# Kernel tuning notes

Hardware: AMD Instinct MI355X
Metric: run time of the kernel (lower is better)

Reference implementation:

```python
import jax, jax.numpy as jnp
import numpy as np

EPS_GN = 1e-5
EPS_ATTN = 1e-6
HEADS = 4
DIM_HEAD = 32
GROUPS = 32  # min(32, channels=128)


def group_norm(x, weight, bias, groups=GROUPS, eps=EPS_GN):
    # x: [b, c, h, w]
    b, c, h, w = x.shape
    xg = x.reshape(b, groups, c // groups, h, w)
    mean = xg.mean(axis=(2, 3, 4), keepdims=True)
    var = xg.var(axis=(2, 3, 4), keepdims=True)
    xg = (xg - mean) * jax.lax.rsqrt(var + eps)
    x = xg.reshape(b, c, h, w)
    return x * weight[None, :, None, None] + bias[None, :, None, None]


def conv1x1(x, w):
    # x: [b, c, h, w], w: [out, in] -> [b, out, h, w]
    return jnp.einsum('bchw,oc->bohw', x, w)


def setup_inputs() -> dict:
    key = jax.random.key(0)
    ks = jax.random.split(key, 6)
    b, c, h, w = 16, 128, 128, 128
    inner = HEADS * DIM_HEAD  # 128
    x = jax.random.normal(ks[0], (b, c, h, w), dtype=jnp.float32)
    gn1_w = jnp.ones((c,), jnp.float32) + 0.02 * jax.random.normal(ks[1], (c,), jnp.float32)
    gn1_b = 0.02 * jax.random.normal(ks[2], (c,), jnp.float32)
    w_qkv = jax.random.normal(ks[3], (inner * 3, c), jnp.float32) / np.sqrt(c)
    w_out = jax.random.normal(ks[4], (c, inner), jnp.float32) / np.sqrt(inner)
    gn2_w = jnp.ones((c,), jnp.float32) + 0.02 * jax.random.normal(ks[5], (c,), jnp.float32)
    gn2_b = jnp.zeros((c,), jnp.float32)
    return {"x": x, "gn1_w": gn1_w, "gn1_b": gn1_b, "w_qkv": w_qkv,
            "w_out": w_out, "gn2_w": gn2_w, "gn2_b": gn2_b}


def reference(x, gn1_w, gn1_b, w_qkv, w_out, gn2_w, gn2_b):
    b, c, h, w = x.shape
    residual = x
    xn = group_norm(x, gn1_w, gn1_b)
    qkv = conv1x1(xn, w_qkv)                      # [b, 3*inner, h, w]
    q, k, v = jnp.split(qkv, 3, axis=1)
    # 'b (heads d) h w -> b heads (h w) d'
    def to_tokens(t):
        return t.reshape(b, HEADS, DIM_HEAD, h * w).transpose(0, 1, 3, 2)
    q, k, v = to_tokens(q), to_tokens(k), to_tokens(v)
    q = jax.nn.elu(q) + 1.0
    k = jax.nn.elu(k) + 1.0
    k_sum = k.sum(axis=2)                          # [b, heads, d]
    kv = jnp.einsum('bhnd,bhne->bhde', k, v)       # [b, heads, d, d]
    qk_sum = jnp.einsum('bhnd,bhd->bhn', q, k_sum) # [b, heads, n]
    qkv_out = jnp.einsum('bhnd,bhde->bhne', q, kv) # [b, heads, n, d]
    out = qkv_out / (qk_sum[..., None] + EPS_ATTN)
    # 'b heads (h w) d -> b (heads d) h w'
    out = out.transpose(0, 1, 3, 2).reshape(b, HEADS * DIM_HEAD, h, w)
    out = conv1x1(out, w_out)
    out = group_norm(out, gn2_w, gn2_b)
    return out + residual
```

## Files before the change

### kernel.cpp

```cpp
#include <hip/hip_runtime.h>

#define B_   16
#define C_   128
#define HW_  16384

typedef __attribute__((ext_vector_type(4))) float  floatx4;
typedef __attribute__((ext_vector_type(8))) short  short8;
typedef __attribute__((ext_vector_type(4))) short  short4v;

static __device__ __forceinline__ unsigned short f2bf(float f){
  unsigned int u = __float_as_uint(f);
  u += 0x7FFFu + ((u >> 16) & 1u);
  return (unsigned short)(u >> 16);
}
static __device__ __forceinline__ float bf2f(unsigned short h){
  return __uint_as_float(((unsigned int)h) << 16);
}
static __device__ __forceinline__ float elu1(float v){
  return v > 0.f ? v + 1.f : __expf(v);
}
static __device__ __forceinline__ int keyx(int n){ return ((n >> 1) & 7) ^ ((n >> 4) & 7); }

__global__ __launch_bounds__(512) void k_xprep(const float* __restrict__ x,
    unsigned short* __restrict__ xT, float* __restrict__ gn1part){
  int blk = blockIdx.x;
  int b = blk >> 6, tile = blk & 63;
  int n0 = tile * 256;
  __shared__ unsigned short XS[32768];
  int t = threadIdx.x, w = t >> 6, l = t & 63;
  float sk[4], sk2[4];
  #pragma unroll
  for (int k = 0; k < 4; ++k){ sk[k] = 0.f; sk2[k] = 0.f; }
  #pragma unroll
  for (int k = 0; k < 4; ++k){
    float4 f4[4];
    #pragma unroll
    for (int j = 0; j < 4; ++j){
      int c = 16*w + 4*k + j;
      f4[j] = *(const float4*)(x + ((size_t)(b*128 + c))*HW_ + n0 + 4*l);
    }
    #pragma unroll
    for (int j = 0; j < 4; ++j){
      sk[k]  += f4[j].x + f4[j].y + f4[j].z + f4[j].w;
      sk2[k] += f4[j].x*f4[j].x + f4[j].y*f4[j].y + f4[j].z*f4[j].z + f4[j].w*f4[j].w;
    }
    int c0 = 16*w + 4*k, cs = c0 >> 3, co = c0 & 7;
    #pragma unroll
    for (int i = 0; i < 4; ++i){
      int n = 4*l + i;
      short4v p;
      #pragma unroll
      for (int j = 0; j < 4; ++j) p[j] = (short)f2bf(((const float*)&f4[j])[i]);
      *(short4v*)(XS + n*128 + (((cs ^ keyx(n)) << 3) + co)) = p;
    }
  }
  #pragma unroll
  for (int k = 0; k < 4; ++k){
    float a = sk[k], q = sk2[k];
    #pragma unroll
    for (int o = 32; o; o >>= 1){ a += __shfl_down(a, o); q += __shfl_down(q, o); }
    if (l == 0){
      gn1part[((size_t)blk)*64 + (4*w + k)*2 + 0] = a;
      gn1part[((size_t)blk)*64 + (4*w + k)*2 + 1] = q;
    }
  }
  __syncthreads();
  unsigned short* dst = xT + ((size_t)blk)*32768;
  for (int it = 0; it < 8; ++it){
    int slot = t + it*512;
    *(short8*)(dst + slot*8) = *(const short8*)(XS + slot*8);
  }
}

__global__ __launch_bounds__(64) void k_gn1fin(const float* __restrict__ gn1part,
    float* __restrict__ mean, float* __restrict__ rstd){
  int bg = blockIdx.x;
  int b = bg >> 5, g = bg & 31, l = threadIdx.x;
  const float* p = gn1part + ((size_t)(b*64 + l))*64 + g*2;
  float s = p[0], s2 = p[1];
  #pragma unroll
  for (int o = 32; o; o >>= 1){ s += __shfl_down(s, o); s2 += __shfl_down(s2, o); }
  if (l == 0){
    float m = s * (1.f/65536.f);
    float var = s2 * (1.f/65536.f) - m*m;
    mean[bg] = m; rstd[bg] = rsqrtf(var + 1e-5f);
  }
}

__global__ __launch_bounds__(64) void k_fold(const float* __restrict__ wqkv, const float* __restrict__ wout,
    const float* __restrict__ g1w, const float* __restrict__ g1b,
    const float* __restrict__ mean, const float* __restrict__ rstd,
    unsigned short* __restrict__ wqp, float* __restrict__ bias, unsigned short* __restrict__ woutb){
  int i = blockIdx.x, l = threadIdx.x;
  if (i < 6144){
    int b = i / 384, o = i % 384;
    float bsum = 0.f;
    #pragma unroll
    for (int j = 0; j < 2; ++j){
      int c = l*2 + j, g = c >> 2;
      float m = mean[b*32 + g], r = rstd[b*32 + g];
      float A  = r * g1w[c];
      float Bc = g1b[c] - m * A;
      float wv = wqkv[o*128 + c];
      wqp[((size_t)(b*384 + o))*128 + c] = f2bf(wv * A);
      bsum += wv * Bc;
    }
    #pragma unroll
    for (int o2 = 32; o2; o2 >>= 1) bsum += __shfl_down(bsum, o2);
    if (l == 0) bias[b*384 + o] = bsum;
  } else {
    int r = i - 6144;
    #pragma unroll
    for (int j = 0; j < 2; ++j){ int c = l*2 + j; woutb[r*128 + c] = f2bf(wout[r*128 + c]); }
  }
}

__global__ __launch_bounds__(512) void k_kv(const unsigned short* __restrict__ xT,
    const unsigned short* __restrict__ wqp, const float* __restrict__ bias,
    float* __restrict__ kvpart, float* __restrict__ ksumpart){
  int blk = blockIdx.x;
  int b = blk >> 7, nt = blk & 127;
  __shared__ unsigned short S[32768];
  int t = threadIdx.x, w = t >> 6, lane = t & 63, lr = lane & 15, lk = lane >> 4;
  const unsigned short* src = xT + ((size_t)(b*64 + (nt >> 1)))*32768 + (nt & 1)*16384;
  for (int it = 0; it < 4; ++it){
    int slot = t + it*512;
    *(short8*)(S + slot*8) = *(const short8*)(src + slot*8);
  }
  __syncthreads();
  short8 afr[2][4]; float biasr[2][4];
  #pragma unroll
  for (int rt = 0; rt < 2; ++rt){
    int o = 128 + rt*128 + w*16;
    #pragma unroll
    for (int ks = 0; ks < 4; ++ks)
      afr[rt][ks] = *(const short8*)(wqp + ((size_t)(b*384 + o + lr))*128 + ks*32 + lk*8);
    #pragma unroll
    for (int r = 0; r < 4; ++r) biasr[rt][r] = bias[b*384 + o + lk*4 + r];
  }
  short4v kpk[8], vpk[8];
  for (int ct = 0; ct < 8; ++ct){
    int nr = ct*16 + lr;
    int kn = keyx(nr);
    short8 bfr[4];
    #pragma unroll
    for (int ks = 0; ks < 4; ++ks)
      bfr[ks] = *(const short8*)(S + nr*128 + (((ks*4 + lk) ^ kn) << 3));
    #pragma unroll
    for (int rt = 0; rt < 2; ++rt){
      floatx4 acc = {0.f,0.f,0.f,0.f};
      #pragma unroll
      for (int ks = 0; ks < 4; ++ks)
        acc = __builtin_amdgcn_mfma_f32_16x16x32_bf16(afr[rt][ks], bfr[ks], acc, 0,0,0);
      short4v pk;
      #pragma unroll
      for (int r = 0; r < 4; ++r){
        float v = acc[r] + biasr[rt][r];
        if (rt == 0) v = elu1(v);
        pk[r] = (short)f2bf(v);
      }
      if (rt == 0) kpk[ct] = pk; else vpk[ct] = pk;
    }
  }
  __syncthreads();
  for (int ct = 0; ct < 8; ++ct){
    int n = ct*16 + lr;
    #pragma unroll
    for (int r = 0; r < 4; ++r){
      int c = w*16 + lk*4 + r;
      int key = (c >> 1) & 7;
      int off = c*128 + ((((n >> 3) ^ key) << 3) + (n & 7));
      S[off]         = (unsigned short)kpk[ct][r];
      S[16384 + off] = (unsigned short)vpk[ct][r];
    }
  }
  __syncthreads();
  short8 ones;
  #pragma unroll
  for (int j = 0; j < 8; ++j) ones[j] = (short)0x3F80;
  #pragma unroll
  for (int j = 0; j < 2; ++j){
    int m = w + 8*j;
    int h = m >> 2, dt = (m >> 1) & 1, et = m & 1;
    int arow = h*32 + dt*16 + lr, brow = h*32 + et*16 + lr;
    int akey = (lr >> 1) & 7;
    floatx4 acc = {0.f,0.f,0.f,0.f}, ks_acc = {0.f,0.f,0.f,0.f};
    #pragma unroll
    for (int ks = 0; ks < 4; ++ks){
      short8 ka = *(const short8*)(S + arow*128 + (((ks*4 + lk) ^ akey) << 3));
      short8 vb = *(const short8*)(S + 16384 + brow*128 + (((ks*4 + lk) ^ akey) << 3));
      acc = __builtin_amdgcn_mfma_f32_16x16x32_bf16(ka, vb, acc, 0,0,0);
      if (et == 0) ks_acc = __builtin_amdgcn_mfma_f32_16x16x32_bf16(ka, ones, ks_acc, 0,0,0);
    }
    float* kvp = kvpart + ((size_t)((b*128 + nt)*4 + h))*1024;
    #pragma unroll
    for (int r = 0; r < 4; ++r)
      kvp[(dt*16 + lk*4 + r)*32 + et*16 + lr] = acc[r];
    if (et == 0 && lr == 0){
      float* ksp = ksumpart + ((size_t)((b*128 + nt)*4 + h))*32;
      #pragma unroll
      for (int r = 0; r < 4; ++r) ksp[dt*16 + lk*4 + r] = ks_acc[r];
    }
  }
}

__global__ __launch_bounds__(256) void k_kvmfold(const float* __restrict__ kvpart, const float* __restrict__ ksumpart,
    const unsigned short* __restrict__ woutb, unsigned short* __restrict__ Mb, float* __restrict__ ksumF){
  int bh = blockIdx.x, t = threadIdx.x;
  int b = bh >> 2, h = bh & 3;
  __shared__ float kvL[1024];
  for (int i = t; i < 1024; i += 256){
    float s = 0.f;
    for (int nt = 0; nt < 128; ++nt) s += kvpart[((size_t)((b*128 + nt)*4 + h))*1024 + i];
    kvL[i] = s;
  }
  if (t < 32){
    float s = 0.f;
    for (int nt = 0; nt < 128; ++nt) s += ksumpart[((size_t)((b*128 + nt)*4 + h))*32 + t];
    ksumF[b*128 + h*32 + t] = s;
  }
  __syncthreads();
  int o = t >> 1, d0 = (t & 1)*16;
  float w2row[32];
  #pragma unroll
  for (int e = 0; e < 32; ++e) w2row[e] = bf2f(woutb[o*128 + h*32 + e]);
  for (int dd = 0; dd < 16; ++dd){
    int d = d0 + dd;
    float s = 0.f;
    #pragma unroll
    for (int e = 0; e < 32; ++e) s += w2row[e] * kvL[d*32 + e];
    Mb[((size_t)b)*16384 + o*128 + h*32 + d] = f2bf(s);
  }
}

__global__ __launch_bounds__(512) void k_attn2(const unsigned short* __restrict__ xT,
    const unsigned short* __restrict__ wqp, const float* __restrict__ bias,
    const float* __restrict__ ksumF, const unsigned short* __restrict__ Mb,
    unsigned short* __restrict__ hbT, float* __restrict__ gn2part){
  int blk = blockIdx.x;
  int b = blk >> 6;
  __shared__ unsigned short S[32768];
  int t = threadIdx.x, w = t >> 6, lane = t & 63, lr = lane & 15, lk = lane >> 4;
  int rg = w & 3, cg = w >> 2;
  const unsigned short* src = xT + ((size_t)blk)*32768;
  for (int it = 0; it < 8; ++it){
    int slot = t + it*512;
    *(short8*)(S + slot*8) = *(const short8*)(src + slot*8);
  }
  short8 afr[2][4]; float biasq[2][4], ksL[2][4];
  #pragma unroll
  for (int rtl = 0; rtl < 2; ++rtl){
    int o = rg*32 + rtl*16;
    #pragma unroll
    for (int ks = 0; ks < 4; ++ks)
      afr[rtl][ks] = *(const short8*)(wqp + ((size_t)(b*384 + o + lr))*128 + ks*32 + lk*8);
    #pragma unroll
    for (int r = 0; r < 4; ++r){
      biasq[rtl][r] = bias[b*384 + o + lk*4 + r];
      ksL[rtl][r]   = ksumF[b*128 + o + lk*4 + r];
    }
  }
  __syncthreads();
  short4v qpk[2][8];
  for (int ct = 0; ct < 8; ++ct){
    int nr = cg*128 + ct*16 + lr;
    int kn = keyx(nr);
    short8 bfr[4];
    #pragma unroll
    for (int ks = 0; ks < 4; ++ks)
      bfr[ks] = *(const short8*)(S + nr*128 + (((ks*4 + lk) ^ kn) << 3));
    float qv[2][4];
    #pragma unroll
    for (int rtl = 0; rtl < 2; ++rtl){
      floatx4 acc = {0.f,0.f,0.f,0.f};
      #pragma unroll
      for (int ks = 0; ks < 4; ++ks)
        acc = __builtin_amdgcn_mfma_f32_16x16x32_bf16(afr[rtl][ks], bfr[ks], acc, 0,0,0);
      #pragma unroll
      for (int r = 0; r < 4; ++r) qv[rtl][r] = elu1(acc[r] + biasq[rtl][r]);
    }
    float p = 0.f;
    #pragma unroll
    for (int rtl = 0; rtl < 2; ++rtl)
      #pragma unroll
      for (int r = 0; r < 4; ++r) p += ksL[rtl][r] * qv[rtl][r];
    p += __shfl_xor(p, 16);
    p += __shfl_xor(p, 32);
    float inv = 1.f / (p + 1e-6f);
    #pragma unroll
    for (int rtl = 0; rtl < 2; ++rtl){
      short4v pk;
      #pragma unroll
      for (int r = 0; r < 4; ++r) pk[r] = (short)f2bf(qv[rtl][r] * inv);
      qpk[rtl][ct] = pk;
    }
  }
  short8 afr2[4];
  #pragma unroll
  for (int ks = 0; ks < 4; ++ks)
    afr2[ks] = *(const short8*)(Mb + ((size_t)b)*16384 + (size_t)(w*16 + lr)*128 + ks*32 + lk*8);
  __syncthreads();
  #pragma unroll
  for (int rtl = 0; rtl < 2; ++rtl){
    int c0 = rg*32 + rtl*16 + lk*4;
    #pragma unroll
    for (int ct = 0; ct < 8; ++ct){
      int n = cg*128 + ct*16 + lr;
      *(short4v*)(S + n*128 + ((((c0 >> 3) ^ (n & 7)) << 3) + (c0 & 7))) = qpk[rtl][ct];
    }
  }
  __syncthreads();
  unsigned short* hdst = hbT + ((size_t)blk)*32768;
  float gs[4] = {0,0,0,0}, gq[4] = {0,0,0,0};
  for (int ct = 0; ct < 16; ++ct){
    int nr = ct*16 + lr;
    short8 bfr[4];
    #pragma unroll
    for (int ks = 0; ks < 4; ++ks)
      bfr[ks] = *(const short8*)(S + nr*128 + (((ks*4 + lk) ^ (nr & 7)) << 3));
    floatx4 acc = {0.f,0.f,0.f,0.f};
    #pragma unroll
    for (int ks = 0; ks < 4; ++ks)
      acc = __builtin_amdgcn_mfma_f32_16x16x32_bf16(afr2[ks], bfr[ks], acc, 0,0,0);
    short4v pk;
    #pragma unroll
    for (int r = 0; r < 4; ++r){
      float hv = acc[r];
      pk[r] = (short)f2bf(hv);
      gs[r] += hv; gq[r] += hv*hv;
    }
    *(short4v*)(hdst + (w*16 + ct)*256 + lane*4) = pk;
  }
  #pragma unroll
  for (int m = 1; m < 16; m <<= 1)
    #pragma unroll
    for (int r = 0; r < 4; ++r){ gs[r] += __shfl_xor(gs[r], m); gq[r] += __shfl_xor(gq[r], m); }
  if (lr == 0){
    #pragma unroll
    for (int r = 0; r < 4; ++r){
      int c = w*16 + lk*4 + r;
      gn2part[((size_t)blk*128 + c)*2 + 0] = gs[r];
      gn2part[((size_t)blk*128 + c)*2 + 1] = gq[r];
    }
  }
}

__global__ __launch_bounds__(64) void k_gn2stats(const float* __restrict__ gn2part,
    float* __restrict__ mean, float* __restrict__ rstd){
  int b = blockIdx.x >> 5, g = blockIdx.x & 31;
  int lane = threadIdx.x;
  float s = 0.f, s2 = 0.f;
  #pragma unroll
  for (int j = 0; j < 4; ++j){
    const float* p = gn2part + (((size_t)(b*64 + lane))*128 + g*4 + j)*2;
    s += p[0]; s2 += p[1];
  }
  #pragma unroll
  for (int o = 32; o; o >>= 1){ s += __shfl_down(s, o); s2 += __shfl_down(s2, o); }
  if (lane == 0){
    float m = s * (1.f/65536.f);
    float var = s2 * (1.f/65536.f) - m*m;
    mean[blockIdx.x] = m; rstd[blockIdx.x] = rsqrtf(var + 1e-5f);
  }
}

__global__ __launch_bounds__(256) void k_final(const unsigned short* __restrict__ hbT,
    const unsigned short* __restrict__ xT, float* __restrict__ out,
    const float* __restrict__ mean, const float* __restrict__ rstd,
    const float* __restrict__ g2w, const float* __restrict__ g2b){
  int blk = blockIdx.x;
  int b = blk >> 7, t128 = blk & 127;
  int tile = t128 >> 1, half = t128 & 1;
  __shared__ unsigned short HS[16384];
  __shared__ unsigned short XS[16384];
  int t = threadIdx.x;
  const unsigned short* hsrc = hbT + ((size_t)(b*64 + tile))*32768;
  const unsigned short* xsrc = xT + ((size_t)(b*64 + tile))*32768 + half*16384;
  for (int it = 0; it < 8; ++it){
    int slot = t + it*256;
    int w8 = slot >> 8, rest = slot & 255;
    *(short8*)(HS + slot*8) = *(const short8*)(hsrc + ((w8*16 + half*8)*256 + rest*8));
    *(short8*)(XS + slot*8) = *(const short8*)(xsrc + slot*8);
  }
  __syncthreads();
  for (int it = 0; it < 8; ++it){
    int idx = t + it*256;
    int c = idx >> 4, oct = idx & 15;
    int bg = b*32 + (c >> 2);
    float m = mean[bg], r = rstd[bg];
    float sc = r * g2w[c], sh = g2b[c] - m * sc;
    int hbase0 = ((c >> 4)*8 + (oct >> 1))*256 + ((c >> 2) & 3)*64 + (oct & 1)*32 + (c & 3);
    float ov[8];
    #pragma unroll
    for (int j = 0; j < 8; ++j){
      int n = oct*8 + j;
      float hv = bf2f(HS[hbase0 + j*4]);
      unsigned short xv = XS[n*128 + ((((c >> 3) ^ keyx(n)) << 3) + (c & 7))];
      ov[j] = hv*sc + sh + bf2f(xv);
    }
    float* op = out + ((size_t)(b*128 + c))*HW_ + t128*128 + oct*8;
    float4 o0, o1;
    o0.x = ov[0]; o0.y = ov[1]; o0.z = ov[2]; o0.w = ov[3];
    o1.x = ov[4]; o1.y = ov[5]; o1.z = ov[6]; o1.w = ov[7];
    *(float4*)op = o0; *(float4*)(op + 4) = o1;
  }
}

extern "C" void kernel_launch(void* const* d_in, const int* in_sizes, int n_in,
                              void* d_out, int out_size, void* d_ws, size_t ws_size,
                              hipStream_t stream){
  const float* x    = (const float*)d_in[0];
  const float* g1w  = (const float*)d_in[1];
  const float* g1b  = (const float*)d_in[2];
  const float* wqkv = (const float*)d_in[3];
  const float* wout = (const float*)d_in[4];
  const float* g2w  = (const float*)d_in[5];
  const float* g2b  = (const float*)d_in[6];
  char* ws = (char*)d_ws;
  (void)in_sizes; (void)n_in; (void)out_size; (void)ws_size;

  float* gn1part  = (float*)(ws + 0);
  float* gn1_mean = (float*)(ws + 262144);
  float* gn1_rstd = (float*)(ws + 264192);
  float* gn2_mean = (float*)(ws + 266240);
  float* gn2_rstd = (float*)(ws + 268288);
  float* bias     = (float*)(ws + 270336);
  unsigned short* woutb = (unsigned short*)(ws + 294912);
  float* ksumF    = (float*)(ws + 327680);
  unsigned short* Mb = (unsigned short*)(ws + 335872);
  unsigned short* wqp = (unsigned short*)(ws + 860160);
  float* ksumpart = (float*)(ws + 2433024);
  float* kvpart   = (float*)(ws + 4194304);
  float* gn2part  = (float*)(ws + 37748736);
  unsigned short* xT  = (unsigned short*)(ws + 46137344);
  unsigned short* hbT = (unsigned short*)(ws + 113246208);

  k_xprep<<<dim3(1024), dim3(512), 0, stream>>>(x, xT, gn1part);
  k_gn1fin<<<dim3(512), dim3(64), 0, stream>>>(gn1part, gn1_mean, gn1_rstd);
  k_fold<<<dim3(6272), dim3(64), 0, stream>>>(wqkv, wout, g1w, g1b, gn1_mean, gn1_rstd, wqp, bias, woutb);
  k_kv<<<dim3(2048), dim3(512), 0, stream>>>(xT, wqp, bias, kvpart, ksumpart);
  k_kvmfold<<<dim3(64), dim3(256), 0, stream>>>(kvpart, ksumpart, woutb, Mb, ksumF);
  k_attn2<<<dim3(1024), dim3(512), 0, stream>>>(xT, wqp, bias, ksumF, Mb, hbT, gn2part);
  k_gn2stats<<<dim3(512), dim3(64), 0, stream>>>(gn2part, gn2_mean, gn2_rstd);
  k_final<<<dim3(2048), dim3(256), 0, stream>>>(hbT, xT, (float*)d_out, gn2_mean, gn2_rstd, g2w, g2b);
}
```

Baseline: 216.5 us.

## Process two token halves per k_kv block and retile attn2 output projection

k_kv now handles a full 256-token tile per block, looping over two halves and accumulating kv and ksum in registers. This halves the grid and the partial buffers that k_kvmfold must reduce. The MFMA operand order is swapped so results are written to LDS as packed short4 stores instead of scalar stores. In k_attn2 each wave now computes two 16-channel row tiles over half the tokens, reusing each LDS B-fragment for two MFMAs. gn2 partials are split by cg, and k_gn2stats is updated to match.

```diff
diff --git a/kernel.cpp b/kernel.cpp
--- a/kernel.cpp
+++ b/kernel.cpp
@@ -119,87 +119,97 @@
     const unsigned short* __restrict__ wqp, const float* __restrict__ bias,
     float* __restrict__ kvpart, float* __restrict__ ksumpart){
   int blk = blockIdx.x;
-  int b = blk >> 7, nt = blk & 127;
+  int b = blk >> 6;
   __shared__ unsigned short S[32768];
   int t = threadIdx.x, w = t >> 6, lane = t & 63, lr = lane & 15, lk = lane >> 4;
-  const unsigned short* src = xT + ((size_t)(b*64 + (nt >> 1)))*32768 + (nt & 1)*16384;
-  for (int it = 0; it < 4; ++it){
-    int slot = t + it*512;
-    *(short8*)(S + slot*8) = *(const short8*)(src + slot*8);
-  }
-  __syncthreads();
-  short8 afr[2][4]; float biasr[2][4];
+  short8 wfr[2][4]; float biasv[2];
   #pragma unroll
   for (int rt = 0; rt < 2; ++rt){
     int o = 128 + rt*128 + w*16;
     #pragma unroll
     for (int ks = 0; ks < 4; ++ks)
-      afr[rt][ks] = *(const short8*)(wqp + ((size_t)(b*384 + o + lr))*128 + ks*32 + lk*8);
-    #pragma unroll
-    for (int r = 0; r < 4; ++r) biasr[rt][r] = bias[b*384 + o + lk*4 + r];
-  }
-  short4v kpk[8], vpk[8];
-  for (int ct = 0; ct < 8; ++ct){
-    int nr = ct*16 + lr;
-    int kn = keyx(nr);
-    short8 bfr[4];
-    #pragma unroll
-    for (int ks = 0; ks < 4; ++ks)
-      bfr[ks] = *(const short8*)(S + nr*128 + (((ks*4 + lk) ^ kn) << 3));
-    #pragma unroll
-    for (int rt = 0; rt < 2; ++rt){
-      floatx4 acc = {0.f,0.f,0.f,0.f};
+      wfr[rt][ks] = *(const short8*)(wqp + ((size_t)(b*384 + o + lr))*128 + ks*32 + lk*8);
+    biasv[rt] = bias[b*384 + o + lr];
+  }
+  short8 ones;
+  #pragma unroll
+  for (int j = 0; j < 8; ++j) ones[j] = (short)0x3F80;
+  floatx4 accA = {0,0,0,0}, accB = {0,0,0,0}, ksaA = {0,0,0,0}, ksaB = {0,0,0,0};
+  for (int half = 0; half < 2; ++half){
+    const unsigned short* src = xT + ((size_t)blk)*32768 + half*16384;
+    for (int it = 0; it < 4; ++it){
+      int slot = t + it*512;
+      *(short8*)(S + slot*8) = *(const short8*)(src + slot*8);
+    }
+    __syncthreads();
+    short4v kpk[8], vpk[8];
+    for (int ct = 0; ct < 8; ++ct){
+      int nr = ct*16 + lr;
+      int kn = keyx(nr);
+      short8 xfr[4];
       #pragma unroll
       for (int ks = 0; ks < 4; ++ks)
-        acc = __builtin_amdgcn_mfma_f32_16x16x32_bf16(afr[rt][ks], bfr[ks], acc, 0,0,0);
-      short4v pk;
-      #pragma unroll
-      for (int r = 0; r < 4; ++r){
-        float v = acc[r] + biasr[rt][r];
-        if (rt == 0) v = elu1(v);
-        pk[r] = (short)f2bf(v);
+        xfr[ks] = *(const short8*)(S + nr*128 + (((ks*4 + lk) ^ kn) << 3));
+      #pragma unroll
+      for (int rt = 0; rt < 2; ++rt){
+        floatx4 acc = {0.f,0.f,0.f,0.f};
+        #pragma unroll
+        for (int ks = 0; ks < 4; ++ks)
+          acc = __builtin_amdgcn_mfma_f32_16x16x32_bf16(xfr[ks], wfr[rt][ks], acc, 0,0,0);
+        short4v pk;
+        #pragma unroll
+        for (int r = 0; r < 4; ++r){
+          float v = acc[r] + biasv[rt];
+          if (rt == 0) v = elu1(v);
+          pk[r] = (short)f2bf(v);
+        }
+        if (rt == 0) kpk[ct] = pk; else vpk[ct] = pk;
       }
-      if (rt == 0) kpk[ct] = pk; else vpk[ct] = pk;
-    }
-  }
-  __syncthreads();
-  for (int ct = 0; ct < 8; ++ct){
-    int n = ct*16 + lr;
-    #pragma unroll
-    for (int r = 0; r < 4; ++r){
-      int c = w*16 + lk*4 + r;
-      int key = (c >> 1) & 7;
-      int off = c*128 + ((((n >> 3) ^ key) << 3) + (n & 7));
-      S[off]         = (unsigned short)kpk[ct][r];
-      S[16384 + off] = (unsigned short)vpk[ct][r];
-    }
-  }
-  __syncthreads();
-  short8 ones;
-  #pragma unroll
-  for (int j = 0; j < 8; ++j) ones[j] = (short)0x3F80;
+    }
+    __syncthreads();
+    #pragma unroll
+    for (int ct = 0; ct < 8; ++ct){
+      int cimg = w*16 + lr;
+      int n0 = ct*16 + lk*4;
+      int off = cimg*128 + ((((n0 >> 3) ^ ((cimg >> 1) & 7)) << 3) + (n0 & 7));
+      *(short4v*)(S + off)         = kpk[ct];
+      *(short4v*)(S + 16384 + off) = vpk[ct];
+    }
+    __syncthreads();
+    #pragma unroll
+    for (int j = 0; j < 2; ++j){
+      int m = w + 8*j;
+      int h = m >> 2, dt = (m >> 1) & 1, et = m & 1;
+      int arow = h*32 + dt*16 + lr, brow = h*32 + et*16 + lr;
+      int akey = (lr >> 1) & 7;
+      #pragma unroll
+      for (int ks = 0; ks < 4; ++ks){
+        short8 ka = *(const short8*)(S + arow*128 + (((ks*4 + lk) ^ akey) << 3));
+        short8 vb = *(const short8*)(S + 16384 + brow*128 + (((ks*4 + lk) ^ akey) << 3));
+        if (j == 0){
+          accA = __builtin_amdgcn_mfma_f32_16x16x32_bf16(ka, vb, accA, 0,0,0);
+          if (et == 0) ksaA = __builtin_amdgcn_mfma_f32_16x16x32_bf16(ka, ones, ksaA, 0,0,0);
+        } else {
+          accB = __builtin_amdgcn_mfma_f32_16x16x32_bf16(ka, vb, accB, 0,0,0);
+          if (et == 0) ksaB = __builtin_amdgcn_mfma_f32_16x16x32_bf16(ka, ones, ksaB, 0,0,0);
+        }
+      }
+    }
+    __syncthreads();
+  }
   #pragma unroll
   for (int j = 0; j < 2; ++j){
     int m = w + 8*j;
     int h = m >> 2, dt = (m >> 1) & 1, et = m & 1;
-    int arow = h*32 + dt*16 + lr, brow = h*32 + et*16 + lr;
-    int akey = (lr >> 1) & 7;
-    floatx4 acc = {0.f,0.f,0.f,0.f}, ks_acc = {0.f,0.f,0.f,0.f};
-    #pragma unroll
-    for (int ks = 0; ks < 4; ++ks){
-      short8 ka = *(const short8*)(S + arow*128 + (((ks*4 + lk) ^ akey) << 3));
-      short8 vb = *(const short8*)(S + 16384 + brow*128 + (((ks*4 + lk) ^ akey) << 3));
-      acc = __builtin_amdgcn_mfma_f32_16x16x32_bf16(ka, vb, acc, 0,0,0);
-      if (et == 0) ks_acc = __builtin_amdgcn_mfma_f32_16x16x32_bf16(ka, ones, ks_acc, 0,0,0);
-    }
-    float* kvp = kvpart + ((size_t)((b*128 + nt)*4 + h))*1024;
+    floatx4 acc = j ? accB : accA, ksa = j ? ksaB : ksaA;
+    float* kvp = kvpart + ((size_t)(blk*4 + h))*1024;
     #pragma unroll
     for (int r = 0; r < 4; ++r)
       kvp[(dt*16 + lk*4 + r)*32 + et*16 + lr] = acc[r];
     if (et == 0 && lr == 0){
-      float* ksp = ksumpart + ((size_t)((b*128 + nt)*4 + h))*32;
-      #pragma unroll
-      for (int r = 0; r < 4; ++r) ksp[dt*16 + lk*4 + r] = ks_acc[r];
+      float* ksp = ksumpart + ((size_t)(blk*4 + h))*32;
+      #pragma unroll
+      for (int r = 0; r < 4; ++r) ksp[dt*16 + lk*4 + r] = ksa[r];
     }
   }
 }
@@ -211,12 +221,12 @@
   __shared__ float kvL[1024];
   for (int i = t; i < 1024; i += 256){
     float s = 0.f;
-    for (int nt = 0; nt < 128; ++nt) s += kvpart[((size_t)((b*128 + nt)*4 + h))*1024 + i];
+    for (int nt = 0; nt < 64; ++nt) s += kvpart[((size_t)((b*64 + nt)*4 + h))*1024 + i];
     kvL[i] = s;
   }
   if (t < 32){
     float s = 0.f;
-    for (int nt = 0; nt < 128; ++nt) s += ksumpart[((size_t)((b*128 + nt)*4 + h))*32 + t];
+    for (int nt = 0; nt < 64; ++nt) s += ksumpart[((size_t)((b*64 + nt)*4 + h))*32 + t];
     ksumF[b*128 + h*32 + t] = s;
   }
   __syncthreads();
@@ -295,10 +305,12 @@
       qpk[rtl][ct] = pk;
     }
   }
-  short8 afr2[4];
-  #pragma unroll
-  for (int ks = 0; ks < 4; ++ks)
-    afr2[ks] = *(const short8*)(Mb + ((size_t)b)*16384 + (size_t)(w*16 + lr)*128 + ks*32 + lk*8);
+  short8 afr2[2][4];
+  #pragma unroll
+  for (int rtl = 0; rtl < 2; ++rtl)
+    #pragma unroll
+    for (int ks = 0; ks < 4; ++ks)
+      afr2[rtl][ks] = *(const short8*)(Mb + ((size_t)b)*16384 + (size_t)((rg*2 + rtl)*16 + lr)*128 + ks*32 + lk*8);
   __syncthreads();
   #pragma unroll
   for (int rtl = 0; rtl < 2; ++rtl){
@@ -311,37 +323,48 @@
   }
   __syncthreads();
   unsigned short* hdst = hbT + ((size_t)blk)*32768;
-  float gs[4] = {0,0,0,0}, gq[4] = {0,0,0,0};
-  for (int ct = 0; ct < 16; ++ct){
-    int nr = ct*16 + lr;
+  float gs[2][4], gq[2][4];
+  #pragma unroll
+  for (int rtl = 0; rtl < 2; ++rtl)
+    #pragma unroll
+    for (int r = 0; r < 4; ++r){ gs[rtl][r] = 0.f; gq[rtl][r] = 0.f; }
+  for (int ct = 0; ct < 8; ++ct){
+    int nr = cg*128 + ct*16 + lr;
     short8 bfr[4];
     #pragma unroll
     for (int ks = 0; ks < 4; ++ks)
       bfr[ks] = *(const short8*)(S + nr*128 + (((ks*4 + lk) ^ (nr & 7)) << 3));
-    floatx4 acc = {0.f,0.f,0.f,0.f};
-    #pragma unroll
-    for (int ks = 0; ks < 4; ++ks)
-      acc = __builtin_amdgcn_mfma_f32_16x16x32_bf16(afr2[ks], bfr[ks], acc, 0,0,0);
-    short4v pk;
-    #pragma unroll
-    for (int r = 0; r < 4; ++r){
-      float hv = acc[r];
-      pk[r] = (short)f2bf(hv);
-      gs[r] += hv; gq[r] += hv*hv;
-    }
-    *(short4v*)(hdst + (w*16 + ct)*256 + lane*4) = pk;
+    #pragma unroll
+    for (int rtl = 0; rtl < 2; ++rtl){
+      floatx4 acc = {0.f,0.f,0.f,0.f};
+      #pragma unroll
+      for (int ks = 0; ks < 4; ++ks)
+        acc = __builtin_amdgcn_mfma_f32_16x16x32_bf16(afr2[rtl][ks], bfr[ks], acc, 0,0,0);
+      short4v pk;
+      #pragma unroll
+      for (int r = 0; r < 4; ++r){
+        float hv = acc[r];
+        pk[r] = (short)f2bf(hv);
+        gs[rtl][r] += hv; gq[rtl][r] += hv*hv;
+      }
+      *(short4v*)(hdst + (((rg*2 + rtl)*16 + cg*8 + ct)*256 + lane*4)) = pk;
+    }
   }
   #pragma unroll
   for (int m = 1; m < 16; m <<= 1)
     #pragma unroll
-    for (int r = 0; r < 4; ++r){ gs[r] += __shfl_xor(gs[r], m); gq[r] += __shfl_xor(gq[r], m); }
+    for (int rtl = 0; rtl < 2; ++rtl)
+      #pragma unroll
+      for (int r = 0; r < 4; ++r){ gs[rtl][r] += __shfl_xor(gs[rtl][r], m); gq[rtl][r] += __shfl_xor(gq[rtl][r], m); }
   if (lr == 0){
     #pragma unroll
-    for (int r = 0; r < 4; ++r){
-      int c = w*16 + lk*4 + r;
-      gn2part[((size_t)blk*128 + c)*2 + 0] = gs[r];
-      gn2part[((size_t)blk*128 + c)*2 + 1] = gq[r];
-    }
+    for (int rtl = 0; rtl < 2; ++rtl)
+      #pragma unroll
+      for (int r = 0; r < 4; ++r){
+        int c = (rg*2 + rtl)*16 + lk*4 + r;
+        gn2part[((size_t)(blk*2 + cg)*128 + c)*2 + 0] = gs[rtl][r];
+        gn2part[((size_t)(blk*2 + cg)*128 + c)*2 + 1] = gq[rtl][r];
+      }
   }
 }
 
@@ -351,10 +374,12 @@
   int lane = threadIdx.x;
   float s = 0.f, s2 = 0.f;
   #pragma unroll
-  for (int j = 0; j < 4; ++j){
-    const float* p = gn2part + (((size_t)(b*64 + lane))*128 + g*4 + j)*2;
-    s += p[0]; s2 += p[1];
-  }
+  for (int cgi = 0; cgi < 2; ++cgi)
+    #pragma unroll
+    for (int j = 0; j < 4; ++j){
+      const float* p = gn2part + ((size_t)(((b*64 + lane)*2 + cgi)*128 + g*4 + j))*2;
+      s += p[0]; s2 += p[1];
+    }
   #pragma unroll
   for (int o = 32; o; o >>= 1){ s += __shfl_down(s, o); s2 += __shfl_down(s2, o); }
   if (lane == 0){
@@ -438,7 +463,7 @@
   k_xprep<<<dim3(1024), dim3(512), 0, stream>>>(x, xT, gn1part);
   k_gn1fin<<<dim3(512), dim3(64), 0, stream>>>(gn1part, gn1_mean, gn1_rstd);
   k_fold<<<dim3(6272), dim3(64), 0, stream>>>(wqkv, wout, g1w, g1b, gn1_mean, gn1_rstd, wqp, bias, woutb);
-  k_kv<<<dim3(2048), dim3(512), 0, stream>>>(xT, wqp, bias, kvpart, ksumpart);
+  k_kv<<<dim3(1024), dim3(512), 0, stream>>>(xT, wqp, bias, kvpart, ksumpart);
   k_kvmfold<<<dim3(64), dim3(256), 0, stream>>>(kvpart, ksumpart, woutb, Mb, ksumF);
   k_attn2<<<dim3(1024), dim3(512), 0, stream>>>(xT, wqp, bias, ksumF, Mb, hbT, gn2part);
   k_gn2stats<<<dim3(512), dim3(64), 0, stream>>>(gn2part, gn2_mean, gn2_rstd);
```

Result: no change. 220.8 us (+2.0%).
